# Optimization experiments

Measured on AMD Instinct MI355X. Metric: run time of the kernel, lower is better.

## Reference

```python
import jax, jax.numpy as jnp
import numpy as np
import math

CH = 256
HEADS = 4
GROUPS = 8
EPS = 1e-5


def group_norm(x, gamma, beta):
    # x: [B, C, H, W], normalize over (C//G, H, W) per group
    B, C, H, W = x.shape
    xg = x.reshape(B, GROUPS, C // GROUPS, H, W)
    mean = xg.mean(axis=(2, 3, 4), keepdims=True)
    var = xg.var(axis=(2, 3, 4), keepdims=True)
    xn = ((xg - mean) * jax.lax.rsqrt(var + EPS)).reshape(B, C, H, W)
    return xn * gamma[None, :, None, None] + beta[None, :, None, None]


def setup_inputs() -> dict:
    key = jax.random.key(0)
    ks = jax.random.split(key, 7)
    B, C, H, W = 4, CH, 64, 64
    x = jax.random.normal(ks[0], (B, C, H, W), dtype=jnp.float32)
    norm_w = jnp.ones((C,), dtype=jnp.float32)
    norm_b = jnp.zeros((C,), dtype=jnp.float32)
    s = 1.0 / math.sqrt(C)
    qkv_w = jax.random.normal(ks[1], (3 * C, C), dtype=jnp.float32) * s  # 1x1 conv kernel
    qkv_b = jnp.zeros((3 * C,), dtype=jnp.float32)
    proj_w = jax.random.normal(ks[2], (C, C), dtype=jnp.float32) * s
    proj_b = jnp.zeros((C,), dtype=jnp.float32)
    return {"x": x, "norm_w": norm_w, "norm_b": norm_b,
            "qkv_w": qkv_w, "qkv_b": qkv_b,
            "proj_w": proj_w, "proj_b": proj_b}


def reference(x, norm_w, norm_b, qkv_w, qkv_b, proj_w, proj_b):
    B, C, H, W = x.shape
    d = C // HEADS
    h = group_norm(x, norm_w, norm_b)
    # 1x1 conv == channel matmul
    qkv = jnp.einsum('oc,bchw->bohw', qkv_w, h) + qkv_b[None, :, None, None]
    qkv = qkv.reshape(B, 3, HEADS, d, H * W)
    q, k, v = qkv[:, 0], qkv[:, 1], qkv[:, 2]  # [B, heads, d, HW]
    attn = jnp.einsum('bhdi,bhdj->bhij', q, k) / jnp.sqrt(jnp.float32(d))
    attn = jax.nn.softmax(attn, axis=-1)
    out = jnp.einsum('bhij,bhdj->bhdi', attn, v).reshape(B, C, H, W)
    out = jnp.einsum('oc,bchw->bohw', proj_w, out) + proj_b[None, :, None, None]
    return x + out
```

## Files before the change

kernel.cpp:

```cpp
#include <hip/hip_runtime.h>
#include <stdint.h>

#define NB    4
#define CC    256
#define NN    4096
#define NHEAD 4
#define DH    64
#define NGRP  8
#define GSIZE 131072

typedef unsigned short u16;
typedef __attribute__((ext_vector_type(8))) short s16x8;
typedef __attribute__((ext_vector_type(4))) float f32x4;

__device__ __forceinline__ u16 f2b(float f) {
  uint32_t x = __float_as_uint(f);
  x += 0x7fffu + ((x >> 16) & 1u);
  return (u16)(x >> 16);
}

__device__ __forceinline__ uint32_t pk2(float a, float b) {
  uint32_t r;
  asm("v_cvt_pk_bf16_f32 %0, %1, %2" : "=v"(r) : "v"(a), "v"(b));
  return r;
}

__global__ __launch_bounds__(256) void k_prep(const float* __restrict__ qw,
                                              const float* __restrict__ pw,
                                              u16* __restrict__ qwb,
                                              u16* __restrict__ pwb,
                                              float* __restrict__ stats) {
  int i = blockIdx.x * 256 + threadIdx.x;
  if (i < 64) stats[i] = 0.f;
  for (int idx = i; idx < 3 * CC * CC; idx += 65536) qwb[idx] = f2b(qw[idx]);
  if (i < CC * CC) pwb[i] = f2b(pw[i]);
}

__global__ __launch_bounds__(256) void k_gn_stats(const float* __restrict__ x,
                                                  float* __restrict__ stats) {
  int grp = blockIdx.x >> 4, sub = blockIdx.x & 15;
  const float4* p4 = (const float4*)(x + (size_t)grp * GSIZE + (size_t)sub * 8192);
  float s = 0.f, s2 = 0.f;
#pragma unroll
  for (int i = 0; i < 8; ++i) {
    float4 v = p4[threadIdx.x + 256 * i];
    s  += v.x + v.y + v.z + v.w;
    s2 += v.x * v.x + v.y * v.y + v.z * v.z + v.w * v.w;
  }
#pragma unroll
  for (int off = 1; off < 64; off <<= 1) { s += __shfl_xor(s, off); s2 += __shfl_xor(s2, off); }
  __shared__ float red[8];
  int w = threadIdx.x >> 6;
  if ((threadIdx.x & 63) == 0) { red[w] = s; red[4 + w] = s2; }
  __syncthreads();
  if (threadIdx.x == 0) {
    s  = red[0] + red[1] + red[2] + red[3];
    s2 = red[4] + red[5] + red[6] + red[7];
    atomicAdd(&stats[grp], s);
    atomicAdd(&stats[32 + grp], s2);
  }
}

__global__ __launch_bounds__(256) void k_gn_norm(const float* __restrict__ x,
                                                 const float* __restrict__ stats,
                                                 const float* __restrict__ gw,
                                                 const float* __restrict__ gb,
                                                 u16* __restrict__ ht) {
  __shared__ u16 T[64 * 72];
  int b = blockIdx.z, cb = blockIdx.y, nb = blockIdx.x;
  int t = threadIdx.x;
  int c = t >> 2, nch = (t & 3) * 16;
  int cg = cb * 64 + c;
  int grp = b * NGRP + (cg >> 5);
  float mean = stats[grp] * (1.f / (float)GSIZE);
  float var  = stats[32 + grp] * (1.f / (float)GSIZE) - mean * mean;
  float rstd = rsqrtf(var + 1e-5f);
  float ga = gw[cg] * rstd;
  float be = gb[cg] - mean * ga;
  const float* px = x + ((size_t)b * CC + cg) * NN + nb * 64 + nch;
#pragma unroll
  for (int k = 0; k < 4; ++k) {
    float4 v = *(const float4*)(px + 4 * k);
    int nl = nch + 4 * k;
    T[(nl + 0) * 72 + c] = f2b(v.x * ga + be);
    T[(nl + 1) * 72 + c] = f2b(v.y * ga + be);
    T[(nl + 2) * 72 + c] = f2b(v.z * ga + be);
    T[(nl + 3) * 72 + c] = f2b(v.w * ga + be);
  }
  __syncthreads();
  int n = t >> 2, cch = (t & 3) * 16;
  u16* dst = ht + ((size_t)b * NN + nb * 64 + n) * CC + cb * 64 + cch;
  *(uint4*)(dst)     = *(const uint4*)&T[n * 72 + cch];
  *(uint4*)(dst + 8) = *(const uint4*)&T[n * 72 + cch + 8];
}

__global__ __launch_bounds__(256) void k_qkv(const u16* __restrict__ Aw,
                                             const float* __restrict__ bias,
                                             const u16* __restrict__ ht,
                                             u16* __restrict__ Qt,
                                             u16* __restrict__ Kt,
                                             u16* __restrict__ Vv) {
  __shared__ u16 sm[5120];
  u16* As = sm;
  u16* Bs = sm + 2560;
  int b = blockIdx.z, bm = blockIdx.y, bn = blockIdx.x;
  int t = threadIdx.x, w = t >> 6, lane = t & 63, lr = lane & 15, lg = lane >> 4;
  int wm = w >> 1, wn = w & 1;
  int srow = t >> 2, sch = (t & 3) * 8;
  const u16* Ap = Aw + (size_t)(bm * 64 + srow) * CC + sch;
  const u16* Bp = ht + ((size_t)b * NN + bn * 64 + srow) * CC + sch;
  f32x4 acc[2][2] = {};
  for (int kt = 0; kt < CC / 32; ++kt) {
    *(uint4*)&As[srow * 40 + sch] = *(const uint4*)(Ap + kt * 32);
    *(uint4*)&Bs[srow * 40 + sch] = *(const uint4*)(Bp + kt * 32);
    __syncthreads();
    s16x8 af[2], bf[2];
#pragma unroll
    for (int fm = 0; fm < 2; ++fm) af[fm] = *(const s16x8*)&As[(wm * 32 + fm * 16 + lr) * 40 + lg * 8];
#pragma unroll
    for (int fn = 0; fn < 2; ++fn) bf[fn] = *(const s16x8*)&Bs[(wn * 32 + fn * 16 + lr) * 40 + lg * 8];
#pragma unroll
    for (int fm = 0; fm < 2; ++fm)
#pragma unroll
      for (int fn = 0; fn < 2; ++fn)
        acc[fm][fn] = __builtin_amdgcn_mfma_f32_16x16x32_bf16(af[fm], bf[fn], acc[fm][fn], 0, 0, 0);
    __syncthreads();
  }
  int which = bm >> 2, head = bm & 3;
  if (which == 2) {
#pragma unroll
    for (int fm = 0; fm < 2; ++fm)
#pragma unroll
      for (int fn = 0; fn < 2; ++fn)
#pragma unroll
        for (int r = 0; r < 4; ++r) {
          int m = wm * 32 + fm * 16 + lg * 4 + r;
          int n = wn * 32 + fn * 16 + lr;
          float v = acc[fm][fn][r] + bias[bm * 64 + m];
          Vv[((size_t)(b * NHEAD + head) * DH + m) * NN + bn * 64 + n] = f2b(v);
        }
  } else {
    u16* Ts = sm;
    float scale = (which == 0) ? 0.125f * 1.44269504f : 1.0f;
#pragma unroll
    for (int fm = 0; fm < 2; ++fm)
#pragma unroll
      for (int fn = 0; fn < 2; ++fn)
#pragma unroll
        for (int r = 0; r < 4; ++r) {
          int m = wm * 32 + fm * 16 + lg * 4 + r;
          int n = wn * 32 + fn * 16 + lr;
          float v = (acc[fm][fn][r] + bias[bm * 64 + m]) * scale;
          Ts[n * 72 + m] = f2b(v);
        }
    __syncthreads();
    u16* dst = (which == 0 ? Qt : Kt);
    int n = t >> 2, cch = (t & 3) * 16;
    u16* o = dst + ((size_t)(b * NHEAD + head) * NN + bn * 64 + n) * DH + cch;
    *(uint4*)(o)     = *(const uint4*)&Ts[n * 72 + cch];
    *(uint4*)(o + 8) = *(const uint4*)&Ts[n * 72 + cch + 8];
  }
}

__global__ __launch_bounds__(256, 2) void k_attn(const u16* __restrict__ Qt,
                                                 const u16* __restrict__ Kt,
                                                 const u16* __restrict__ Vv,
                                                 u16* __restrict__ att) {
  __shared__ __align__(16) u16 Ks[128 * 72];
  __shared__ __align__(16) u16 Vs[64 * 136];
  int bh = blockIdx.y, qt = blockIdx.x;
  int t = threadIdx.x, w = t >> 6, lane = t & 63, lr = lane & 15, lg = lane >> 4;
  const u16* Qb = Qt + ((size_t)bh * NN + qt * 128 + w * 32) * DH;
  const u16* Kb = Kt + (size_t)bh * NN * DH;
  const u16* Vb = Vv + (size_t)bh * DH * NN;
  s16x8 bq0[2], bq1[2];
#pragma unroll
  for (int kk = 0; kk < 2; ++kk) {
    bq0[kk] = *(const s16x8*)(Qb + lr * DH + kk * 32 + lg * 8);
    bq1[kk] = *(const s16x8*)(Qb + (16 + lr) * DH + kk * 32 + lg * 8);
  }
  const s16x8 ones = (s16x8)(short)0x3F80;
  float m0 = -1e30f, m1 = -1e30f;
  f32x4 oacc[2][4] = {};
  f32x4 la0 = {}, la1 = {};
  int srK = t >> 1, scK = (t & 1) * 32;
  int wK = srK & 63;
  int prK = (srK & 64) | (wK & 32) | (((wK >> 2) & 3) << 3) | (((wK >> 4) & 1) << 2) | (wK & 3);
  const u16* kp0 = Kb + (size_t)prK * DH + scK;
  u16* ksw = &Ks[srK * 72 + scK];
  int srV = t >> 2, scV = (t & 3) * 32;
  const u16* vp0 = Vb + (size_t)srV * NN + scV;
  u16* vsw = &Vs[srV * 136 + scV];
  {
    uint4 a0 = *(const uint4*)(kp0),      a1 = *(const uint4*)(kp0 + 8);
    uint4 a2 = *(const uint4*)(kp0 + 16), a3 = *(const uint4*)(kp0 + 24);
    uint4 b0 = *(const uint4*)(vp0),      b1 = *(const uint4*)(vp0 + 8);
    uint4 b2 = *(const uint4*)(vp0 + 16), b3 = *(const uint4*)(vp0 + 24);
    *(uint4*)(ksw) = a0; *(uint4*)(ksw + 8) = a1; *(uint4*)(ksw + 16) = a2; *(uint4*)(ksw + 24) = a3;
    *(uint4*)(vsw) = b0; *(uint4*)(vsw + 8) = b1; *(uint4*)(vsw + 16) = b2; *(uint4*)(vsw + 24) = b3;
  }
  __syncthreads();
  for (int j0 = 0; j0 < NN; j0 += 128) {
    int jn = (j0 + 128 < NN) ? j0 + 128 : 0;
    const u16* kp = kp0 + (size_t)jn * DH;
    const u16* vp = vp0 + jn;
    uint4 rka = *(const uint4*)(kp),      rkb = *(const uint4*)(kp + 8);
    uint4 rkc = *(const uint4*)(kp + 16), rkd = *(const uint4*)(kp + 24);
    uint4 rva = *(const uint4*)(vp),      rvb = *(const uint4*)(vp + 8);
    uint4 rvc = *(const uint4*)(vp + 16), rvd = *(const uint4*)(vp + 24);
    f32x4 s0[8], s1[8];
    __builtin_amdgcn_s_setprio(1);
#pragma unroll
    for (int q = 0; q < 8; ++q) {
      const u16* base = &Ks[(q * 16 + lr) * 72 + lg * 8];
      s16x8 a0 = *(const s16x8*)(base);
      s16x8 a1 = *(const s16x8*)(base + 32);
      f32x4 z0 = {}, z1 = {};
      z0 = __builtin_amdgcn_mfma_f32_16x16x32_bf16(a0, bq0[0], z0, 0, 0, 0);
      z1 = __builtin_amdgcn_mfma_f32_16x16x32_bf16(a0, bq1[0], z1, 0, 0, 0);
      z0 = __builtin_amdgcn_mfma_f32_16x16x32_bf16(a1, bq0[1], z0, 0, 0, 0);
      z1 = __builtin_amdgcn_mfma_f32_16x16x32_bf16(a1, bq1[1], z1, 0, 0, 0);
      s0[q] = z0; s1[q] = z1;
    }
    __builtin_amdgcn_s_setprio(0);
    union { s16x8 v; uint32_t u[4]; } pb0[4], pb1[4];
    {
      float mx = fmaxf(s0[0][0], s0[0][1]);
      mx = fmaxf(mx, fmaxf(s0[0][2], s0[0][3]));
#pragma unroll
      for (int q = 1; q < 8; ++q) {
        mx = fmaxf(mx, fmaxf(s0[q][0], s0[q][1]));
        mx = fmaxf(mx, fmaxf(s0[q][2], s0[q][3]));
      }
      mx = fmaxf(mx, __shfl_xor(mx, 16));
      mx = fmaxf(mx, __shfl_xor(mx, 32));
      if (__any(mx > m0 + 8.f)) {
        float mnew  = fmaxf(m0, mx);
        float alpha = exp2f(m0 - mnew);
#pragma unroll
        for (int dt = 0; dt < 4; ++dt)
#pragma unroll
          for (int r = 0; r < 4; ++r) oacc[0][dt][r] *= alpha;
#pragma unroll
        for (int r = 0; r < 4; ++r) la0[r] *= alpha;
        m0 = mnew;
      }
#pragma unroll
      for (int q = 0; q < 8; ++q) {
        float p0 = exp2f(s0[q][0] - m0);
        float p1 = exp2f(s0[q][1] - m0);
        float p2 = exp2f(s0[q][2] - m0);
        float p3 = exp2f(s0[q][3] - m0);
        int c = (q >> 2) * 2 + ((q >> 1) & 1);
        pb0[c].u[(q & 1) * 2]     = pk2(p0, p1);
        pb0[c].u[(q & 1) * 2 + 1] = pk2(p2, p3);
      }
    }
    {
      float mx = fmaxf(s1[0][0], s1[0][1]);
      mx = fmaxf(mx, fmaxf(s1[0][2], s1[0][3]));
#pragma unroll
      for (int q = 1; q < 8; ++q) {
        mx = fmaxf(mx, fmaxf(s1[q][0], s1[q][1]));
        mx = fmaxf(mx, fmaxf(s1[q][2], s1[q][3]));
      }
      mx = fmaxf(mx, __shfl_xor(mx, 16));
      mx = fmaxf(mx, __shfl_xor(mx, 32));
      if (__any(mx > m1 + 8.f)) {
        float mnew  = fmaxf(m1, mx);
        float alpha = exp2f(m1 - mnew);
#pragma unroll
        for (int dt = 0; dt < 4; ++dt)
#pragma unroll
          for (int r = 0; r < 4; ++r) oacc[1][dt][r] *= alpha;
#pragma unroll
        for (int r = 0; r < 4; ++r) la1[r] *= alpha;
        m1 = mnew;
      }
#pragma unroll
      for (int q = 0; q < 8; ++q) {
        float p0 = exp2f(s1[q][0] - m1);
        float p1 = exp2f(s1[q][1] - m1);
        float p2 = exp2f(s1[q][2] - m1);
        float p3 = exp2f(s1[q][3] - m1);
        int c = (q >> 2) * 2 + ((q >> 1) & 1);
        pb1[c].u[(q & 1) * 2]     = pk2(p0, p1);
        pb1[c].u[(q & 1) * 2 + 1] = pk2(p2, p3);
      }
    }
    __builtin_amdgcn_s_setprio(1);
#pragma unroll
    for (int dt = 0; dt < 4; ++dt) {
      const u16* vb2 = &Vs[(dt * 16 + lr) * 136 + lg * 8];
#pragma unroll
      for (int c = 0; c < 4; ++c) {
        s16x8 av = *(const s16x8*)(vb2 + c * 32);
        oacc[0][dt] = __builtin_amdgcn_mfma_f32_16x16x32_bf16(av, pb0[c].v, oacc[0][dt], 0, 0, 0);
        oacc[1][dt] = __builtin_amdgcn_mfma_f32_16x16x32_bf16(av, pb1[c].v, oacc[1][dt], 0, 0, 0);
      }
    }
#pragma unroll
    for (int c = 0; c < 4; ++c) {
      la0 = __builtin_amdgcn_mfma_f32_16x16x32_bf16(ones, pb0[c].v, la0, 0, 0, 0);
      la1 = __builtin_amdgcn_mfma_f32_16x16x32_bf16(ones, pb1[c].v, la1, 0, 0, 0);
    }
    __builtin_amdgcn_s_setprio(0);
    __syncthreads();
    *(uint4*)(ksw) = rka; *(uint4*)(ksw + 8) = rkb; *(uint4*)(ksw + 16) = rkc; *(uint4*)(ksw + 24) = rkd;
    *(uint4*)(vsw) = rva; *(uint4*)(vsw + 8) = rvb; *(uint4*)(vsw + 16) = rvc; *(uint4*)(vsw + 24) = rvd;
    __syncthreads();
  }
  int b = bh >> 2, h = bh & 3;
#pragma unroll
  for (int g = 0; g < 2; ++g) {
    float linv = 1.f / (g ? la1[0] : la0[0]);
    u16* ob = att + ((size_t)b * NN + qt * 128 + w * 32 + g * 16 + lr) * CC + h * 64 + lg * 4;
#pragma unroll
    for (int dt = 0; dt < 4; ++dt) {
      f32x4 oa = oacc[g][dt];
      uint2 pkd;
      pkd.x = pk2(oa[0] * linv, oa[1] * linv);
      pkd.y = pk2(oa[2] * linv, oa[3] * linv);
      *(uint2*)(ob + dt * 16) = pkd;
    }
  }
}

__global__ __launch_bounds__(256) void k_proj(const u16* __restrict__ Aw,
                                              const float* __restrict__ bias,
                                              const u16* __restrict__ att,
                                              const float* __restrict__ x,
                                              float* __restrict__ out) {
  __shared__ u16 sm[5120];
  u16* As = sm;
  u16* Bs = sm + 2560;
  int b = blockIdx.z, bm = blockIdx.y, bn = blockIdx.x;
  int t = threadIdx.x, w = t >> 6, lane = t & 63, lr = lane & 15, lg = lane >> 4;
  int wm = w >> 1, wn = w & 1;
  int srow = t >> 2, sch = (t & 3) * 8;
  const u16* Ap = Aw + (size_t)(bm * 64 + srow) * CC + sch;
  const u16* Bp = att + ((size_t)b * NN + bn * 64 + srow) * CC + sch;
  f32x4 acc[2][2] = {};
  for (int kt = 0; kt < CC / 32; ++kt) {
    *(uint4*)&As[srow * 40 + sch] = *(const uint4*)(Ap + kt * 32);
    *(uint4*)&Bs[srow * 40 + sch] = *(const uint4*)(Bp + kt * 32);
    __syncthreads();
    s16x8 af[2], bf[2];
#pragma unroll
    for (int fm = 0; fm < 2; ++fm) af[fm] = *(const s16x8*)&As[(wm * 32 + fm * 16 + lr) * 40 + lg * 8];
#pragma unroll
    for (int fn = 0; fn < 2; ++fn) bf[fn] = *(const s16x8*)&Bs[(wn * 32 + fn * 16 + lr) * 40 + lg * 8];
#pragma unroll
    for (int fm = 0; fm < 2; ++fm)
#pragma unroll
      for (int fn = 0; fn < 2; ++fn)
        acc[fm][fn] = __builtin_amdgcn_mfma_f32_16x16x32_bf16(af[fm], bf[fn], acc[fm][fn], 0, 0, 0);
    __syncthreads();
  }
#pragma unroll
  for (int fm = 0; fm < 2; ++fm)
#pragma unroll
    for (int fn = 0; fn < 2; ++fn)
#pragma unroll
      for (int r = 0; r < 4; ++r) {
        int o = bm * 64 + wm * 32 + fm * 16 + lg * 4 + r;
        int n = bn * 64 + wn * 32 + fn * 16 + lr;
        size_t idx = ((size_t)b * CC + o) * NN + n;
        out[idx] = x[idx] + bias[o] + acc[fm][fn][r];
      }
}

extern "C" void kernel_launch(void* const* d_in, const int* in_sizes, int n_in,
                              void* d_out, int out_size, void* d_ws, size_t ws_size,
                              hipStream_t stream) {
  const float* x  = (const float*)d_in[0];
  const float* nw = (const float*)d_in[1];
  const float* nb = (const float*)d_in[2];
  const float* qw = (const float*)d_in[3];
  const float* qb = (const float*)d_in[4];
  const float* pw = (const float*)d_in[5];
  const float* pb = (const float*)d_in[6];
  float* out = (float*)d_out;
  char* ws = (char*)d_ws;
  float* stats = (float*)(ws + 0);
  u16* qwb = (u16*)(ws + 4096);
  u16* pwb = (u16*)(ws + 397312);
  u16* ht  = (u16*)(ws + 528384);
  u16* Qt  = (u16*)(ws + 8916992);
  u16* Kt  = (u16*)(ws + 17305600);
  u16* Vv  = (u16*)(ws + 25694208);
  u16* att = (u16*)(ws + 34082816);

  k_prep<<<dim3(256), dim3(256), 0, stream>>>(qw, pw, qwb, pwb, stats);
  k_gn_stats<<<dim3(512), dim3(256), 0, stream>>>(x, stats);
  k_gn_norm<<<dim3(64, 4, NB), dim3(256), 0, stream>>>(x, stats, nw, nb, ht);
  k_qkv<<<dim3(64, 12, NB), dim3(256), 0, stream>>>(qwb, qb, ht, Qt, Kt, Vv);
  k_attn<<<dim3(32, NB * NHEAD), dim3(256), 0, stream>>>(Qt, Kt, Vv, att);
  k_proj<<<dim3(64, 4, NB), dim3(256), 0, stream>>>(pwb, pb, att, x, out);
}
```

Measured before the change: 177.4 us.

## Split attention KV range across two wave groups with in-block softmax merge

The attention kernel now launches 512 threads per block, with two halves each processing half of the key/value sequence for the same 128 queries. The KV tile shrinks from 128 to 64 keys per iteration, and at the end the two partial results (max, sum, accumulators) are merged through shared memory. The aim is more waves per CU to hide latency on a grid of only 512 blocks, at the cost of a final merge step and lower register headroom under launch_bounds(512,4).

After: 165.9 us. -6.5%, faster.

```diff
diff --git a/kernel.cpp b/kernel.cpp
--- a/kernel.cpp
+++ b/kernel.cpp
@@ -162,15 +162,15 @@
   }
 }
 
-__global__ __launch_bounds__(256, 2) void k_attn(const u16* __restrict__ Qt,
+__global__ __launch_bounds__(512, 4) void k_attn(const u16* __restrict__ Qt,
                                                  const u16* __restrict__ Kt,
                                                  const u16* __restrict__ Vv,
                                                  u16* __restrict__ att) {
-  __shared__ __align__(16) u16 Ks[128 * 72];
-  __shared__ __align__(16) u16 Vs[64 * 136];
+  __shared__ __align__(16) u16 sm[18432];
   int bh = blockIdx.y, qt = blockIdx.x;
   int t = threadIdx.x, w = t >> 6, lane = t & 63, lr = lane & 15, lg = lane >> 4;
-  const u16* Qb = Qt + ((size_t)bh * NN + qt * 128 + w * 32) * DH;
+  int wq = w & 3, h = w >> 2;
+  const u16* Qb = Qt + ((size_t)bh * NN + qt * 128 + wq * 32) * DH;
   const u16* Kb = Kt + (size_t)bh * NN * DH;
   const u16* Vb = Vv + (size_t)bh * DH * NN;
   s16x8 bq0[2], bq1[2];
@@ -183,36 +183,34 @@
   float m0 = -1e30f, m1 = -1e30f;
   f32x4 oacc[2][4] = {};
   f32x4 la0 = {}, la1 = {};
-  int srK = t >> 1, scK = (t & 1) * 32;
-  int wK = srK & 63;
-  int prK = (srK & 64) | (wK & 32) | (((wK >> 2) & 3) << 3) | (((wK >> 4) & 1) << 2) | (wK & 3);
-  const u16* kp0 = Kb + (size_t)prK * DH + scK;
-  u16* ksw = &Ks[srK * 72 + scK];
-  int srV = t >> 2, scV = (t & 3) * 32;
-  const u16* vp0 = Vb + (size_t)srV * NN + scV;
-  u16* vsw = &Vs[srV * 136 + scV];
+  u16* Ksh = sm + h * 9216;
+  u16* Vsh = sm + h * 9216 + 4608;
+  int tl = t & 255;
+  int srow = tl >> 2, sch = (tl & 3) * 16;
+  int prow = (srow & 32) | (((srow >> 2) & 3) << 3) | (((srow >> 4) & 1) << 2) | (srow & 3);
+  int jbase = h * 2048;
+  const u16* kp0 = Kb + (size_t)(jbase + prow) * DH + sch;
+  const u16* vp0 = Vb + (size_t)srow * NN + jbase + sch;
+  u16* ksw = Ksh + srow * 72 + sch;
+  u16* vsw = Vsh + srow * 72 + sch;
   {
-    uint4 a0 = *(const uint4*)(kp0),      a1 = *(const uint4*)(kp0 + 8);
-    uint4 a2 = *(const uint4*)(kp0 + 16), a3 = *(const uint4*)(kp0 + 24);
-    uint4 b0 = *(const uint4*)(vp0),      b1 = *(const uint4*)(vp0 + 8);
-    uint4 b2 = *(const uint4*)(vp0 + 16), b3 = *(const uint4*)(vp0 + 24);
-    *(uint4*)(ksw) = a0; *(uint4*)(ksw + 8) = a1; *(uint4*)(ksw + 16) = a2; *(uint4*)(ksw + 24) = a3;
-    *(uint4*)(vsw) = b0; *(uint4*)(vsw + 8) = b1; *(uint4*)(vsw + 16) = b2; *(uint4*)(vsw + 24) = b3;
+    uint4 a0 = *(const uint4*)(kp0), a1 = *(const uint4*)(kp0 + 8);
+    uint4 b0 = *(const uint4*)(vp0), b1 = *(const uint4*)(vp0 + 8);
+    *(uint4*)(ksw) = a0; *(uint4*)(ksw + 8) = a1;
+    *(uint4*)(vsw) = b0; *(uint4*)(vsw + 8) = b1;
   }
   __syncthreads();
-  for (int j0 = 0; j0 < NN; j0 += 128) {
-    int jn = (j0 + 128 < NN) ? j0 + 128 : 0;
+  for (int j0 = 0; j0 < 2048; j0 += 64) {
+    int jn = (j0 + 64 < 2048) ? j0 + 64 : 0;
     const u16* kp = kp0 + (size_t)jn * DH;
     const u16* vp = vp0 + jn;
-    uint4 rka = *(const uint4*)(kp),      rkb = *(const uint4*)(kp + 8);
-    uint4 rkc = *(const uint4*)(kp + 16), rkd = *(const uint4*)(kp + 24);
-    uint4 rva = *(const uint4*)(vp),      rvb = *(const uint4*)(vp + 8);
-    uint4 rvc = *(const uint4*)(vp + 16), rvd = *(const uint4*)(vp + 24);
-    f32x4 s0[8], s1[8];
+    uint4 rka = *(const uint4*)(kp), rkb = *(const uint4*)(kp + 8);
+    uint4 rva = *(const uint4*)(vp), rvb = *(const uint4*)(vp + 8);
+    f32x4 s0[4], s1[4];
     __builtin_amdgcn_s_setprio(1);
 #pragma unroll
-    for (int q = 0; q < 8; ++q) {
-      const u16* base = &Ks[(q * 16 + lr) * 72 + lg * 8];
+    for (int q = 0; q < 4; ++q) {
+      const u16* base = Ksh + (q * 16 + lr) * 72 + lg * 8;
       s16x8 a0 = *(const s16x8*)(base);
       s16x8 a1 = *(const s16x8*)(base + 32);
       f32x4 z0 = {}, z1 = {};
@@ -223,12 +221,12 @@
       s0[q] = z0; s1[q] = z1;
     }
     __builtin_amdgcn_s_setprio(0);
-    union { s16x8 v; uint32_t u[4]; } pb0[4], pb1[4];
+    union { s16x8 v; uint32_t u[4]; } pb0[2], pb1[2];
     {
       float mx = fmaxf(s0[0][0], s0[0][1]);
       mx = fmaxf(mx, fmaxf(s0[0][2], s0[0][3]));
 #pragma unroll
-      for (int q = 1; q < 8; ++q) {
+      for (int q = 1; q < 4; ++q) {
         mx = fmaxf(mx, fmaxf(s0[q][0], s0[q][1]));
         mx = fmaxf(mx, fmaxf(s0[q][2], s0[q][3]));
       }
@@ -246,12 +244,12 @@
         m0 = mnew;
       }
 #pragma unroll
-      for (int q = 0; q < 8; ++q) {
+      for (int q = 0; q < 4; ++q) {
         float p0 = exp2f(s0[q][0] - m0);
         float p1 = exp2f(s0[q][1] - m0);
         float p2 = exp2f(s0[q][2] - m0);
         float p3 = exp2f(s0[q][3] - m0);
-        int c = (q >> 2) * 2 + ((q >> 1) & 1);
+        int c = (q >> 1) & 1;
         pb0[c].u[(q & 1) * 2]     = pk2(p0, p1);
         pb0[c].u[(q & 1) * 2 + 1] = pk2(p2, p3);
       }
@@ -260,7 +258,7 @@
       float mx = fmaxf(s1[0][0], s1[0][1]);
       mx = fmaxf(mx, fmaxf(s1[0][2], s1[0][3]));
 #pragma unroll
-      for (int q = 1; q < 8; ++q) {
+      for (int q = 1; q < 4; ++q) {
         mx = fmaxf(mx, fmaxf(s1[q][0], s1[q][1]));
         mx = fmaxf(mx, fmaxf(s1[q][2], s1[q][3]));
       }
@@ -278,12 +276,12 @@
         m1 = mnew;
       }
 #pragma unroll
-      for (int q = 0; q < 8; ++q) {
+      for (int q = 0; q < 4; ++q) {
         float p0 = exp2f(s1[q][0] - m1);
         float p1 = exp2f(s1[q][1] - m1);
         float p2 = exp2f(s1[q][2] - m1);
         float p3 = exp2f(s1[q][3] - m1);
-        int c = (q >> 2) * 2 + ((q >> 1) & 1);
+        int c = (q >> 1) & 1;
         pb1[c].u[(q & 1) * 2]     = pk2(p0, p1);
         pb1[c].u[(q & 1) * 2 + 1] = pk2(p2, p3);
       }
@@ -291,37 +289,62 @@
     __builtin_amdgcn_s_setprio(1);
 #pragma unroll
     for (int dt = 0; dt < 4; ++dt) {
-      const u16* vb2 = &Vs[(dt * 16 + lr) * 136 + lg * 8];
-#pragma unroll
-      for (int c = 0; c < 4; ++c) {
+      const u16* vb2 = Vsh + (dt * 16 + lr) * 72 + lg * 8;
+#pragma unroll
+      for (int c = 0; c < 2; ++c) {
         s16x8 av = *(const s16x8*)(vb2 + c * 32);
         oacc[0][dt] = __builtin_amdgcn_mfma_f32_16x16x32_bf16(av, pb0[c].v, oacc[0][dt], 0, 0, 0);
         oacc[1][dt] = __builtin_amdgcn_mfma_f32_16x16x32_bf16(av, pb1[c].v, oacc[1][dt], 0, 0, 0);
       }
     }
 #pragma unroll
-    for (int c = 0; c < 4; ++c) {
+    for (int c = 0; c < 2; ++c) {
       la0 = __builtin_amdgcn_mfma_f32_16x16x32_bf16(ones, pb0[c].v, la0, 0, 0, 0);
       la1 = __builtin_amdgcn_mfma_f32_16x16x32_bf16(ones, pb1[c].v, la1, 0, 0, 0);
     }
     __builtin_amdgcn_s_setprio(0);
     __syncthreads();
-    *(uint4*)(ksw) = rka; *(uint4*)(ksw + 8) = rkb; *(uint4*)(ksw + 16) = rkc; *(uint4*)(ksw + 24) = rkd;
-    *(uint4*)(vsw) = rva; *(uint4*)(vsw + 8) = rvb; *(uint4*)(vsw + 16) = rvc; *(uint4*)(vsw + 24) = rvd;
-    __syncthreads();
-  }
-  int b = bh >> 2, h = bh & 3;
-#pragma unroll
-  for (int g = 0; g < 2; ++g) {
-    float linv = 1.f / (g ? la1[0] : la0[0]);
-    u16* ob = att + ((size_t)b * NN + qt * 128 + w * 32 + g * 16 + lr) * CC + h * 64 + lg * 4;
-#pragma unroll
-    for (int dt = 0; dt < 4; ++dt) {
-      f32x4 oa = oacc[g][dt];
-      uint2 pkd;
-      pkd.x = pk2(oa[0] * linv, oa[1] * linv);
-      pkd.y = pk2(oa[2] * linv, oa[3] * linv);
-      *(uint2*)(ob + dt * 16) = pkd;
+    *(uint4*)(ksw) = rka; *(uint4*)(ksw + 8) = rkb;
+    *(uint4*)(vsw) = rva; *(uint4*)(vsw + 8) = rvb;
+    __syncthreads();
+  }
+  float* F = (float*)sm;
+  float* slot = F + (wq * 64 + lane) * 36;
+  if (h == 1) {
+#pragma unroll
+    for (int g = 0; g < 2; ++g)
+#pragma unroll
+      for (int dt = 0; dt < 4; ++dt)
+#pragma unroll
+        for (int r = 0; r < 4; ++r) slot[g * 16 + dt * 4 + r] = oacc[g][dt][r];
+    slot[32] = m0; slot[33] = la0[0];
+    slot[34] = m1; slot[35] = la1[0];
+  }
+  __syncthreads();
+  if (h == 0) {
+    int b = bh >> 2, hd = bh & 3;
+#pragma unroll
+    for (int g = 0; g < 2; ++g) {
+      float mA = g ? m1 : m0;
+      float lA = g ? la1[0] : la0[0];
+      float mB = slot[32 + g * 2];
+      float lB = slot[33 + g * 2];
+      float M  = fmaxf(mA, mB);
+      float aA = exp2f(mA - M);
+      float aB = exp2f(mB - M);
+      float linv = 1.f / (lA * aA + lB * aB);
+      u16* ob = att + ((size_t)b * NN + qt * 128 + wq * 32 + g * 16 + lr) * CC + hd * 64 + lg * 4;
+#pragma unroll
+      for (int dt = 0; dt < 4; ++dt) {
+        float o0 = (oacc[g][dt][0] * aA + slot[g * 16 + dt * 4 + 0] * aB) * linv;
+        float o1 = (oacc[g][dt][1] * aA + slot[g * 16 + dt * 4 + 1] * aB) * linv;
+        float o2 = (oacc[g][dt][2] * aA + slot[g * 16 + dt * 4 + 2] * aB) * linv;
+        float o3 = (oacc[g][dt][3] * aA + slot[g * 16 + dt * 4 + 3] * aB) * linv;
+        uint2 pkd;
+        pkd.x = pk2(o0, o1);
+        pkd.y = pk2(o2, o3);
+        *(uint2*)(ob + dt * 16) = pkd;
+      }
     }
   }
 }
@@ -395,6 +418,6 @@
   k_gn_stats<<<dim3(512), dim3(256), 0, stream>>>(x, stats);
   k_gn_norm<<<dim3(64, 4, NB), dim3(256), 0, stream>>>(x, stats, nw, nb, ht);
   k_qkv<<<dim3(64, 12, NB), dim3(256), 0, stream>>>(qwb, qb, ht, Qt, Kt, Vv);
-  k_attn<<<dim3(32, NB * NHEAD), dim3(256), 0, stream>>>(Qt, Kt, Vv, att);
+  k_attn<<<dim3(32, NB * NHEAD), dim3(512), 0, stream>>>(Qt, Kt, Vv, att);
   k_proj<<<dim3(64, 4, NB), dim3(256), 0, stream>>>(pwb, pb, att, x, out);
 }
```
